# Performance work log

Measured on AMD Instinct MI355X. Metric: run time of the kernel, lower is better.

The kernel has to match this reference:

```python
import jax, jax.numpy as jnp
import numpy as np

B, N, Q, D, H = 8, 2048, 256, 1024, 16
HD = D // H


def setup_inputs() -> dict:
    key = jax.random.key(0)
    ks = jax.random.split(key, 6)
    scale = 1.0 / np.sqrt(D)
    return {
        "sources": jax.random.normal(ks[0], (B, N, D), dtype=jnp.float32),
        "queries": jax.random.normal(ks[1], (B, Q, D), dtype=jnp.float32),
        "w_in": jax.random.normal(ks[2], (3 * D, D), dtype=jnp.float32) * scale,
        "b_in": jax.random.normal(ks[3], (3 * D,), dtype=jnp.float32) * 0.02,
        "w_out": jax.random.normal(ks[4], (D, D), dtype=jnp.float32) * scale,
        "b_out": jax.random.normal(ks[5], (D,), dtype=jnp.float32) * 0.02,
    }


def reference(sources, queries, w_in, b_in, w_out, b_out):
    # torch nn.MultiheadAttention (batch_first, eval mode, no attn_mask),
    # applied per-sample with equal lengths == one batched cross-attention.
    w_q, w_k, w_v = jnp.split(w_in, 3, axis=0)   # each [D, D]
    b_q, b_k, b_v = jnp.split(b_in, 3, axis=0)
    q = queries @ w_q.T + b_q                    # [B, Q, D]
    k = sources @ w_k.T + b_k                    # [B, N, D]
    v = sources @ w_v.T + b_v                    # [B, N, D]
    q = q.reshape(B, Q, H, HD)
    k = k.reshape(B, N, H, HD)
    v = v.reshape(B, N, H, HD)
    scale = 1.0 / np.sqrt(HD).astype(np.float32)
    scores = jnp.einsum("bqhd,bkhd->bhqk", q, k) * scale  # [B, H, Q, N]
    attn = jax.nn.softmax(scores, axis=-1)
    out = jnp.einsum("bhqk,bkhd->bqhd", attn, v).reshape(B, Q, D)
    out = out @ w_out.T + b_out                  # out_proj
    return out + queries                         # residual (fix=False: no norm)
```

## Files before the change

### kernel.cpp

```cpp
#include <hip/hip_runtime.h>
#include <hip/hip_bf16.h>


typedef unsigned short u16;
typedef __attribute__((ext_vector_type(8))) short short8;
typedef __attribute__((ext_vector_type(4))) float floatx4;

static_assert(sizeof(short8) == 16, "short8 must be 16B");

__device__ __forceinline__ u16 f2bf(float f) {
  unsigned int x = __float_as_uint(f);
  x += 0x7fffu + ((x >> 16) & 1u);
  return (u16)(x >> 16);
}

__device__ __forceinline__ void gload16(const u16* g, u16* lds) {
  __builtin_amdgcn_global_load_lds(
      (const __attribute__((address_space(1))) unsigned int*)g,
      (__attribute__((address_space(3))) unsigned int*)lds, 16, 0, 0);
}

template <int N> __device__ __forceinline__ void vmwait() {
  if constexpr (N == 0)      asm volatile("s_waitcnt vmcnt(0)" ::: "memory");
  else if constexpr (N == 4) asm volatile("s_waitcnt vmcnt(4)" ::: "memory");
  else if constexpr (N == 6) asm volatile("s_waitcnt vmcnt(6)" ::: "memory");
  else if constexpr (N == 8) asm volatile("s_waitcnt vmcnt(8)" ::: "memory");
  else static_assert(N == 0, "unsupported vmcnt immediate");
}

__device__ __forceinline__ void lgkm0() {
  asm volatile("s_waitcnt lgkmcnt(0)" ::: "memory");
}

__device__ __forceinline__ void sfence() { __builtin_amdgcn_sched_barrier(0); }

__global__ __launch_bounds__(256) void f2bf_multi(
    const float* __restrict__ s, u16* __restrict__ so,
    const float* __restrict__ q, u16* __restrict__ qo,
    const float* __restrict__ wi, u16* __restrict__ wio,
    const float* __restrict__ wo, u16* __restrict__ woo) {
  int i = blockIdx.x * 256 + threadIdx.x;
  const float* in; u16* out; int idx;
  if (i < 4194304)      { in = s;  out = so;  idx = i; }
  else if (i < 4718592) { in = q;  out = qo;  idx = i - 4194304; }
  else if (i < 5505024) { in = wi; out = wio; idx = i - 4718592; }
  else if (i < 5767168) { in = wo; out = woo; idx = i - 5505024; }
  else return;
  float4 v = reinterpret_cast<const float4*>(in)[idx];
  ushort4 o;
  o.x = f2bf(v.x); o.y = f2bf(v.y); o.z = f2bf(v.z); o.w = f2bf(v.w);
  reinterpret_cast<ushort4*>(out)[idx] = o;
}

template <int MT, int NT>
__device__ __forceinline__ void gemm_core(
    const u16* __restrict__ A, int lda,
    const u16* __restrict__ Bm, int ldb, int K,
    u16* __restrict__ Alds, u16* __restrict__ Blds,
    floatx4 (&acc)[MT][NT]) {
  const int t = threadIdx.x;
  const int wave = t >> 6, lane = t & 63;
  const int rr = lane & 15, kq = lane >> 4;
  constexpr int AI = MT, BI = NT;
  constexpr int AELEMS = MT * 32 * 64;
  constexpr int BELEMS = NT * 32 * 64;

  const u16* ag[AI]; u16* al[AI];
#pragma unroll
  for (int i = 0; i < AI; ++i) {
    int s = i * 256 + t;
    int row = s >> 3, c16 = s & 7;
    ag[i] = A + (size_t)row * lda + ((c16 ^ (row & 7)) * 8);
    al[i] = Alds + (size_t)(i * 256 + wave * 64) * 8;
  }
  const u16* bg[BI]; u16* blp[BI];
#pragma unroll
  for (int i = 0; i < BI; ++i) {
    int s = i * 256 + t;
    int row = s >> 3, c16 = s & 7;
    bg[i] = Bm + (size_t)row * ldb + ((c16 ^ (row & 7)) * 8);
    blp[i] = Blds + (size_t)(i * 256 + wave * 64) * 8;
  }

  const int m0w = (wave & 1) * (MT * 16);
  const int n0w = (wave >> 1) * (NT * 16);
  int aoff[MT][2], boff[NT][2];
#pragma unroll
  for (int mi = 0; mi < MT; ++mi) {
    int row = m0w + mi * 16 + rr;
#pragma unroll
    for (int kk = 0; kk < 2; ++kk)
      aoff[mi][kk] = row * 64 + (((kk * 4 + kq) ^ (row & 7)) * 8);
  }
#pragma unroll
  for (int ni = 0; ni < NT; ++ni) {
    int row = n0w + ni * 16 + rr;
#pragma unroll
    for (int kk = 0; kk < 2; ++kk)
      boff[ni][kk] = row * 64 + (((kk * 4 + kq) ^ (row & 7)) * 8);
  }

  auto compute = [&](int bs) {
    const u16* Ab = Alds + bs * AELEMS;
    const u16* Bb = Blds + bs * BELEMS;
#pragma unroll
    for (int kk = 0; kk < 2; ++kk) {
      short8 af[MT], bfr[NT];
#pragma unroll
      for (int mi = 0; mi < MT; ++mi)
        af[mi] = *reinterpret_cast<const short8*>(Ab + aoff[mi][kk]);
#pragma unroll
      for (int ni = 0; ni < NT; ++ni)
        bfr[ni] = *reinterpret_cast<const short8*>(Bb + boff[ni][kk]);
      __builtin_amdgcn_s_setprio(1);
#pragma unroll
      for (int mi = 0; mi < MT; ++mi)
#pragma unroll
        for (int ni = 0; ni < NT; ++ni)
          acc[mi][ni] = __builtin_amdgcn_mfma_f32_16x16x32_bf16(af[mi], bfr[ni], acc[mi][ni], 0, 0, 0);
      __builtin_amdgcn_s_setprio(0);
    }
  };

  const int nt = K >> 6;

#pragma unroll
  for (int i = 0; i < AI; ++i) gload16(ag[i], al[i]);
#pragma unroll
  for (int i = 0; i < BI; ++i) gload16(bg[i], blp[i]);

  int cur = 0;
#pragma unroll 1
  for (int tt = 0; tt < nt - 1; ++tt) {
    const int nxt = cur ^ 1;
    const int koff = (tt + 1) * 64;
#pragma unroll
    for (int i = 0; i < AI; ++i) gload16(ag[i] + koff, al[i] + nxt * AELEMS);
#pragma unroll
    for (int i = 0; i < BI; ++i) gload16(bg[i] + koff, blp[i] + nxt * BELEMS);
    sfence();
    vmwait<AI + BI>();
    __builtin_amdgcn_s_barrier();
    sfence();
    compute(cur);
    sfence();
    __builtin_amdgcn_s_barrier();
    cur = nxt;
  }
  sfence();
  vmwait<0>();
  __builtin_amdgcn_s_barrier();
  sfence();
  compute(cur);
}


template <int LO>
__device__ __forceinline__ void read_a8(const u16* ab, int kcol0, int kcol1,
                                        short8 (&af)[8][2]) {
#pragma unroll
  for (int mi = 0; mi < 4; ++mi) {
    af[LO + mi][0] = *reinterpret_cast<const short8*>(ab + (LO + mi) * 1024 + kcol0);
    af[LO + mi][1] = *reinterpret_cast<const short8*>(ab + (LO + mi) * 1024 + kcol1);
  }
}

template <int LO>
__device__ __forceinline__ void read_b8(const u16* bb, int kcol0, int kcol1,
                                        short8 (&bf)[4][2]) {
#pragma unroll
  for (int ni = 0; ni < 2; ++ni) {
    bf[LO + ni][0] = *reinterpret_cast<const short8*>(bb + (LO + ni) * 1024 + kcol0);
    bf[LO + ni][1] = *reinterpret_cast<const short8*>(bb + (LO + ni) * 1024 + kcol1);
  }
}

template <int M0, int N0>
__device__ __forceinline__ void quad8(const short8 (&af)[8][2], const short8 (&bf)[4][2],
                                      floatx4 (&acc)[8][4]) {
  __builtin_amdgcn_s_setprio(1);
#pragma unroll
  for (int kk = 0; kk < 2; ++kk)
#pragma unroll
    for (int mi = 0; mi < 4; ++mi)
#pragma unroll
      for (int ni = 0; ni < 2; ++ni)
        acc[M0 + mi][N0 + ni] = __builtin_amdgcn_mfma_f32_16x16x32_bf16(
            af[M0 + mi][kk], bf[N0 + ni][kk], acc[M0 + mi][N0 + ni], 0, 0, 0);
  __builtin_amdgcn_s_setprio(0);
}

__global__ __launch_bounds__(512, 2) void gemm_proj_kv8(
    const u16* __restrict__ s_bf, const u16* __restrict__ wi_bf,
    const float* __restrict__ b_in,
    u16* __restrict__ kp, u16* __restrict__ vT) {
  __shared__ __attribute__((aligned(16))) u16 Alds[2 * 256 * 64];
  __shared__ __attribute__((aligned(16))) u16 Blds[2 * 256 * 64];

  int bid = blockIdx.y * 8 + blockIdx.x;
  int nb = (bid & 7) * 64 + (bid >> 3);
  const int by = nb >> 3, bx = nb & 7;
  const int mB = by * 256;
  const int nB = bx * 256;
  const u16* Ag = s_bf + (size_t)mB * 1024;
  const u16* Wg = wi_bf + (size_t)(1024 + nB) * 1024;
  const float* bias = b_in + 1024 + nB;

  const int t = threadIdx.x;
  const int w = t >> 6, lane = t & 63;
  const int rr = lane & 15, kq = lane >> 4;
  const int wr = w >> 2, wc = w & 3;

  const u16* ga[2][2]; const u16* gb[2][2];
#pragma unroll
  for (int h = 0; h < 2; ++h)
#pragma unroll
    for (int i = 0; i < 2; ++i) {
      int s = i * 512 + t;
      int row = h * 128 + (s >> 3), c16 = s & 7;
      ga[h][i] = Ag + (size_t)row * 1024 + ((c16 ^ (row & 7)) * 8);
      gb[h][i] = Wg + (size_t)row * 1024 + ((c16 ^ (row & 7)) * 8);
    }

#define STAGE_A8(j, h) { const int d_ = ((j) & 1) * 16384;                         \
    gload16(ga[h][0] + (size_t)(j) * 64, Alds + d_ + (h) * 8192 + w * 512);        \
    gload16(ga[h][1] + (size_t)(j) * 64, Alds + d_ + (h) * 8192 + 4096 + w * 512); }
#define STAGE_B8(j, h) { const int d_ = ((j) & 1) * 16384;                         \
    gload16(gb[h][0] + (size_t)(j) * 64, Blds + d_ + (h) * 8192 + w * 512);        \
    gload16(gb[h][1] + (size_t)(j) * 64, Blds + d_ + (h) * 8192 + 4096 + w * 512); }

  const int kcol0 = ((kq) ^ (rr & 7)) * 8;
  const int kcol1 = ((4 + kq) ^ (rr & 7)) * 8;
  const u16* abase = Alds + (wr * 128 + rr) * 64;
  const u16* bbase = Blds + (wc * 64 + rr) * 64;

  short8 af[8][2], bf[4][2];
  const floatx4 zz = {0.f, 0.f, 0.f, 0.f};
  floatx4 acc[8][4];
#pragma unroll
  for (int mi = 0; mi < 8; ++mi)
#pragma unroll
    for (int ni = 0; ni < 4; ++ni) acc[mi][ni] = zz;

  STAGE_A8(0, 0); STAGE_B8(0, 0); STAGE_A8(0, 1); STAGE_B8(0, 1);
  STAGE_A8(1, 0); STAGE_B8(1, 0);
  sfence();
  vmwait<4>();
  __builtin_amdgcn_s_barrier();
  sfence();

#pragma unroll 1
  for (int kt = 0; kt < 16; ++kt) {
    const int doff = (kt & 1) * 16384;
    const u16* ab = abase + doff;
    const u16* bb = bbase + doff;
    read_a8<0>(ab, kcol0, kcol1, af);
    read_b8<0>(bb, kcol0, kcol1, bf);
    if (kt + 1 < 16) STAGE_A8(kt + 1, 1);
    sfence();
    __builtin_amdgcn_s_barrier();
    lgkm0(); sfence();
    quad8<0, 0>(af, bf, acc);
    sfence();
    __builtin_amdgcn_s_barrier();
    sfence();
    read_a8<4>(ab, kcol0, kcol1, af);
    read_b8<2>(bb, kcol0, kcol1, bf);
    if (kt + 1 < 16) STAGE_B8(kt + 1, 1);
    sfence();
    __builtin_amdgcn_s_barrier();
    lgkm0(); sfence();
    quad8<0, 2>(af, bf, acc);
    sfence();
    __builtin_amdgcn_s_barrier();
    sfence();
    if (kt + 2 < 16) STAGE_A8(kt + 2, 0);
    sfence();
    __builtin_amdgcn_s_barrier();
    quad8<4, 0>(af, bf, acc);
    sfence();
    __builtin_amdgcn_s_barrier();
    sfence();
    if (kt + 2 < 16) { STAGE_B8(kt + 2, 0); sfence(); vmwait<4>(); }
    else             { sfence(); vmwait<0>(); }
    __builtin_amdgcn_s_barrier();
    quad8<4, 2>(af, bf, acc);
    sfence();
    __builtin_amdgcn_s_barrier();
    sfence();
  }
#undef STAGE_A8
#undef STAGE_B8

  const int r4 = kq * 4;
  const int m0w = wr * 128, n0w = wc * 64;
  if (nB < 1024) {
#pragma unroll
    for (int mi = 0; mi < 8; ++mi)
#pragma unroll
      for (int ni = 0; ni < 4; ++ni) {
        int nl = n0w + ni * 16 + rr;
        float bv = bias[nl];
#pragma unroll
        for (int r = 0; r < 4; ++r) {
          int m = mB + m0w + mi * 16 + r4 + r;
          kp[(size_t)m * 1024 + nB + nl] = f2bf(acc[mi][ni][r] + bv);
        }
      }
  } else {
#pragma unroll
    for (int mi = 0; mi < 8; ++mi)
#pragma unroll
      for (int ni = 0; ni < 4; ++ni) {
        int n2 = nB + n0w + ni * 16 + rr - 1024;
        int h = n2 >> 6, d = n2 & 63;
        float bv = bias[n0w + ni * 16 + rr];
        int m0 = mB + m0w + mi * 16 + r4;
        int b = m0 >> 11, j0 = m0 & 2047;
        ushort4 o;
        o.x = f2bf(acc[mi][ni][0] + bv);
        o.y = f2bf(acc[mi][ni][1] + bv);
        o.z = f2bf(acc[mi][ni][2] + bv);
        o.w = f2bf(acc[mi][ni][3] + bv);
        *reinterpret_cast<ushort4*>(
            vT + ((size_t)(b * 16 + h) * 64 + d) * 2048 + j0) = o;
      }
  }
}

__global__ __launch_bounds__(256, 2) void gemm_proj_q(
    const u16* __restrict__ qy_bf, const u16* __restrict__ wi_bf,
    const float* __restrict__ b_in, u16* __restrict__ qp) {
  __shared__ __attribute__((aligned(16))) u16 Alds[2 * 128 * 64];
  __shared__ __attribute__((aligned(16))) u16 Blds[2 * 128 * 64];
  const int mB = blockIdx.y * 128;
  const int nB = blockIdx.x * 128;
  const u16* A = qy_bf + (size_t)mB * 1024;
  const u16* W = wi_bf + (size_t)nB * 1024;
  const float* bias = b_in + nB;

  const floatx4 zz = {0.f, 0.f, 0.f, 0.f};
  floatx4 acc[4][4] = {{zz, zz, zz, zz}, {zz, zz, zz, zz}, {zz, zz, zz, zz}, {zz, zz, zz, zz}};
  gemm_core<4, 4>(A, 1024, W, 1024, 1024, Alds, Blds, acc);

  const int lane = threadIdx.x & 63, wave = threadIdx.x >> 6;
  const int rr = lane & 15, r4 = (lane >> 4) * 4;
  const int m0w = (wave & 1) * 64, n0w = (wave >> 1) * 64;
#pragma unroll
  for (int mi = 0; mi < 4; ++mi)
#pragma unroll
    for (int ni = 0; ni < 4; ++ni) {
      int nl = n0w + ni * 16 + rr;
      float bv = bias[nl];
#pragma unroll
      for (int r = 0; r < 4; ++r) {
        int m = mB + m0w + mi * 16 + r4 + r;
        qp[(size_t)m * 1024 + nB + nl] = f2bf((acc[mi][ni][r] + bv) * 0.125f);
      }
    }
}

__global__ __launch_bounds__(256, 2) void gemm_scores_exp(
    const u16* __restrict__ qp, const u16* __restrict__ kp,
    u16* __restrict__ sc, int b0) {
  __shared__ __attribute__((aligned(16))) u16 Alds[128 * 64];
  __shared__ __attribute__((aligned(16))) u16 Blds[128 * 64];
  const int bz = blockIdx.z, bl = bz >> 4, h = bz & 15;
  const int b = b0 + bl;
  const int mB = blockIdx.y * 128;
  const int nB = blockIdx.x * 128;
  const u16* A = qp + (size_t)b * 256 * 1024 + h * 64 + (size_t)mB * 1024;
  const u16* Bm = kp + (size_t)b * 2048 * 1024 + h * 64 + (size_t)nB * 1024;
  u16* C = sc + (size_t)bz * 256 * 2048;
  const floatx4 zz = {0.f, 0.f, 0.f, 0.f};
  floatx4 acc[4][4] = {{zz, zz, zz, zz}, {zz, zz, zz, zz}, {zz, zz, zz, zz}, {zz, zz, zz, zz}};
  gemm_core<4, 4>(A, 1024, Bm, 1024, 64, Alds, Blds, acc);

  const int lane = threadIdx.x & 63, wave = threadIdx.x >> 6;
  const int rr = lane & 15, r4 = (lane >> 4) * 4;
  const int m0w = (wave & 1) * 64, n0w = (wave >> 1) * 64;
#pragma unroll
  for (int mi = 0; mi < 4; ++mi)
#pragma unroll
    for (int ni = 0; ni < 4; ++ni) {
      int n = nB + n0w + ni * 16 + rr;
#pragma unroll
      for (int r = 0; r < 4; ++r) {
        int m = mB + m0w + mi * 16 + r4 + r;
        C[(size_t)m * 2048 + n] = f2bf(__expf(acc[mi][ni][r]));
      }
    }
}

__global__ __launch_bounds__(256, 2) void gemm_pv(
    const u16* __restrict__ sc, const u16* __restrict__ vT,
    u16* __restrict__ ao, int b0) {
  __shared__ __attribute__((aligned(16))) u16 Alds[2 * 64 * 64];
  __shared__ __attribute__((aligned(16))) u16 Blds[2 * 64 * 64];
  const int t = threadIdx.x;
  const int wave = t >> 6, lane = t & 63;
  const int rr = lane & 15, kq = lane >> 4;
  const int bz = blockIdx.z, bl = bz >> 4, h = bz & 15;
  const int b = b0 + bl;
  const int mB = blockIdx.y * 64;
  const u16* A = sc + (size_t)bz * 256 * 2048 + (size_t)mB * 2048;
  const u16* Bm = vT + (size_t)(b * 16 + h) * 64 * 2048;

  const u16* ag[2]; u16* al[2]; const u16* bg[2]; u16* blp[2];
#pragma unroll
  for (int i = 0; i < 2; ++i) {
    int s = i * 256 + t, row = s >> 3, c16 = s & 7;
    ag[i] = A + (size_t)row * 2048 + ((c16 ^ (row & 7)) * 8);
    al[i] = Alds + (size_t)(i * 256 + wave * 64) * 8;
    bg[i] = Bm + (size_t)row * 2048 + ((c16 ^ (row & 7)) * 8);
    blp[i] = Blds + (size_t)(i * 256 + wave * 64) * 8;
  }

  const int m0w = (wave & 1) * 32;
  const int n0w = (wave >> 1) * 32;
  int aoff[2][2], boff[2][2];
#pragma unroll
  for (int mi = 0; mi < 2; ++mi) {
    int row = m0w + mi * 16 + rr;
#pragma unroll
    for (int kk = 0; kk < 2; ++kk)
      aoff[mi][kk] = row * 64 + (((kk * 4 + kq) ^ (row & 7)) * 8);
  }
#pragma unroll
  for (int ni = 0; ni < 2; ++ni) {
    int row = n0w + ni * 16 + rr;
#pragma unroll
    for (int kk = 0; kk < 2; ++kk)
      boff[ni][kk] = row * 64 + (((kk * 4 + kq) ^ (row & 7)) * 8);
  }

  const short ov = (rr == 0) ? (short)0x3F80 : (short)0;
  const short8 ones = {ov, ov, ov, ov, ov, ov, ov, ov};

  const floatx4 zz = {0.f, 0.f, 0.f, 0.f};
  floatx4 acc[2][2] = {{zz, zz}, {zz, zz}};
  floatx4 acc_l[2] = {zz, zz};

  auto compute = [&](int bs) {
    const u16* Ab = Alds + bs * 4096;
    const u16* Bb = Blds + bs * 4096;
#pragma unroll
    for (int kk = 0; kk < 2; ++kk) {
      short8 af[2], bfr[2];
#pragma unroll
      for (int mi = 0; mi < 2; ++mi)
        af[mi] = *reinterpret_cast<const short8*>(Ab + aoff[mi][kk]);
#pragma unroll
      for (int ni = 0; ni < 2; ++ni)
        bfr[ni] = *reinterpret_cast<const short8*>(Bb + boff[ni][kk]);
      __builtin_amdgcn_s_setprio(1);
#pragma unroll
      for (int mi = 0; mi < 2; ++mi) {
#pragma unroll
        for (int ni = 0; ni < 2; ++ni)
          acc[mi][ni] = __builtin_amdgcn_mfma_f32_16x16x32_bf16(af[mi], bfr[ni], acc[mi][ni], 0, 0, 0);
        acc_l[mi] = __builtin_amdgcn_mfma_f32_16x16x32_bf16(af[mi], ones, acc_l[mi], 0, 0, 0);
      }
      __builtin_amdgcn_s_setprio(0);
    }
  };

#pragma unroll
  for (int i = 0; i < 2; ++i) gload16(ag[i], al[i]);
#pragma unroll
  for (int i = 0; i < 2; ++i) gload16(bg[i], blp[i]);

  int cur = 0;
#pragma unroll 1
  for (int tt = 0; tt < 31; ++tt) {
    const int nxt = cur ^ 1;
    const int koff = (tt + 1) * 64;
#pragma unroll
    for (int i = 0; i < 2; ++i) gload16(ag[i] + koff, al[i] + nxt * 4096);
#pragma unroll
    for (int i = 0; i < 2; ++i) gload16(bg[i] + koff, blp[i] + nxt * 4096);
    sfence();
    vmwait<4>();
    __builtin_amdgcn_s_barrier();
    sfence();
    compute(cur);
    sfence();
    __builtin_amdgcn_s_barrier();
    cur = nxt;
  }
  sfence();
  vmwait<0>();
  __builtin_amdgcn_s_barrier();
  sfence();
  compute(cur);

#pragma unroll
  for (int mi = 0; mi < 2; ++mi)
#pragma unroll
    for (int r = 0; r < 4; ++r) {
      float l = __shfl(acc_l[mi][r], lane & 48, 64);
      float inv = 1.0f / l;
      int m = mB + m0w + mi * 16 + kq * 4 + r;
#pragma unroll
      for (int ni = 0; ni < 2; ++ni) {
        int n = n0w + ni * 16 + rr;
        ao[(size_t)(b * 256 + m) * 1024 + h * 64 + n] = f2bf(acc[mi][ni][r] * inv);
      }
    }
}

__global__ __launch_bounds__(256, 2) void gemm_out(
    const u16* __restrict__ A, const u16* __restrict__ W,
    const float* __restrict__ bias, const float* __restrict__ resid,
    float* __restrict__ out) {
  __shared__ __attribute__((aligned(16))) u16 Alds[2 * 64 * 64];
  __shared__ __attribute__((aligned(16))) u16 Blds[2 * 128 * 64];
  const int mB = blockIdx.y * 64;
  const int nB = blockIdx.x * 128;
  const floatx4 zz = {0.f, 0.f, 0.f, 0.f};
  floatx4 acc[2][4] = {{zz, zz, zz, zz}, {zz, zz, zz, zz}};
  gemm_core<2, 4>(A + (size_t)mB * 1024, 1024, W + (size_t)nB * 1024, 1024, 1024,
                  Alds, Blds, acc);
  const int lane = threadIdx.x & 63, wave = threadIdx.x >> 6;
  const int rr = lane & 15, r4 = (lane >> 4) * 4;
  const int m0w = (wave & 1) * 32, n0w = (wave >> 1) * 64;
#pragma unroll
  for (int mi = 0; mi < 2; ++mi)
#pragma unroll
    for (int ni = 0; ni < 4; ++ni) {
      int n = nB + n0w + ni * 16 + rr;
      float bv = bias[n];
#pragma unroll
      for (int r = 0; r < 4; ++r) {
        int m = mB + m0w + mi * 16 + r4 + r;
        size_t idx = (size_t)m * 1024 + n;
        out[idx] = acc[mi][ni][r] + bv + resid[idx];
      }
    }
}

extern "C" void kernel_launch(void* const* d_in, const int* in_sizes, int n_in,
                              void* d_out, int out_size, void* d_ws, size_t ws_size,
                              hipStream_t stream) {
  const float* sources = (const float*)d_in[0];
  const float* queries = (const float*)d_in[1];
  const float* w_in    = (const float*)d_in[2];
  const float* b_in    = (const float*)d_in[3];
  const float* w_out   = (const float*)d_in[4];
  const float* b_out   = (const float*)d_in[5];
  float* out = (float*)d_out;

  char* ws = (char*)d_ws;
  size_t off = 0;
  auto alloc = [&](size_t elems) -> u16* {
    u16* p = (u16*)(ws + off);
    off += elems * sizeof(u16);
    off = (off + 255) & ~(size_t)255;
    return p;
  };
  u16* s_bf  = alloc((size_t)16777216);
  u16* qy_bf = alloc((size_t)2097152);
  u16* wi_bf = alloc((size_t)3145728);
  u16* wo_bf = alloc((size_t)1048576);
  u16* qp    = alloc((size_t)2097152);
  u16* kp    = alloc((size_t)16777216);
  u16* vT    = alloc((size_t)16777216);
  u16* ao    = alloc((size_t)2097152);
  const size_t sc_elems_per_b = (size_t)16 * 256 * 2048;
  size_t remain = ws_size > off ? ws_size - off : 0;
  int bchunk = (int)(remain / (sc_elems_per_b * sizeof(u16)));
  if (bchunk > 8) bchunk = 8;
  if (bchunk < 1) bchunk = 1;
  u16* sc = (u16*)(ws + off);

  f2bf_multi<<<dim3(22528), 256, 0, stream>>>(
      sources, s_bf, queries, qy_bf, w_in, wi_bf, w_out, wo_bf);

  gemm_proj_kv8<<<dim3(8, 64), 512, 0, stream>>>(s_bf, wi_bf, b_in, kp, vT);
  gemm_proj_q<<<dim3(8, 16), 256, 0, stream>>>(qy_bf, wi_bf, b_in, qp);

  for (int b0 = 0; b0 < 8; b0 += bchunk) {
    int nb = (8 - b0) < bchunk ? (8 - b0) : bchunk;
    gemm_scores_exp<<<dim3(16, 2, nb * 16), 256, 0, stream>>>(qp, kp, sc, b0);
    gemm_pv<<<dim3(1, 4, nb * 16), 256, 0, stream>>>(sc, vT, ao, b0);
  }

  gemm_out<<<dim3(8, 32), 256, 0, stream>>>(ao, wo_bf, b_out, queries, out);
}
```

Measured before the change: 314.6 us.

## Fuse scores-exp and PV GEMMs into one flash-style attention kernel

Replaces the separate score+exp kernel and the PV kernel, which went through a large bf16 score buffer in global memory, with a single fused kernel. Each block handles a (batch, head, 128-query) tile and streams K/V tiles through double-buffered LDS. Exponentiated scores are staged in LDS and consumed directly by the PV MFMAs, and row sums are reduced across waves at the end. This removes the global write and read of the score matrix and a kernel launch, but keeps the unnormalized exp without max subtraction and leaves only 256 blocks of 512 threads.

```diff
diff --git a/kernel.cpp b/kernel.cpp
--- a/kernel.cpp
+++ b/kernel.cpp
@@ -12,6 +12,10 @@
   unsigned int x = __float_as_uint(f);
   x += 0x7fffu + ((x >> 16) & 1u);
   return (u16)(x >> 16);
+}
+
+__device__ __forceinline__ float bf2f(u16 b) {
+  return __uint_as_float(((unsigned int)b) << 16);
 }
 
 __device__ __forceinline__ void gload16(const u16* g, u16* lds) {
@@ -154,7 +158,6 @@
   compute(cur);
 }
 
-
 template <int LO>
 __device__ __forceinline__ void read_a8(const u16* ab, int kcol0, int kcol1,
                                         short8 (&af)[8][2]) {
@@ -360,151 +363,201 @@
     }
 }
 
-__global__ __launch_bounds__(256, 2) void gemm_scores_exp(
+__global__ __launch_bounds__(512, 2) void attn_fused(
     const u16* __restrict__ qp, const u16* __restrict__ kp,
-    u16* __restrict__ sc, int b0) {
-  __shared__ __attribute__((aligned(16))) u16 Alds[128 * 64];
-  __shared__ __attribute__((aligned(16))) u16 Blds[128 * 64];
-  const int bz = blockIdx.z, bl = bz >> 4, h = bz & 15;
-  const int b = b0 + bl;
-  const int mB = blockIdx.y * 128;
-  const int nB = blockIdx.x * 128;
-  const u16* A = qp + (size_t)b * 256 * 1024 + h * 64 + (size_t)mB * 1024;
-  const u16* Bm = kp + (size_t)b * 2048 * 1024 + h * 64 + (size_t)nB * 1024;
-  u16* C = sc + (size_t)bz * 256 * 2048;
+    const u16* __restrict__ vT, u16* __restrict__ ao) {
+  __shared__ __attribute__((aligned(16))) u16 Qlds[8192];
+  __shared__ __attribute__((aligned(16))) u16 Klds[2][8192];
+  __shared__ __attribute__((aligned(16))) u16 Vlds[2][8192];
+  __shared__ __attribute__((aligned(16))) u16 Plds[16384];
+  __shared__ float l_part[4][128];
+
+  const int bid = blockIdx.x;
+  const int nb = (bid & 7) * 32 + (bid >> 3);
+  const int bh = nb >> 1, qh = nb & 1;
+  const int b = bh >> 4, h = bh & 15;
+
+  const int t = threadIdx.x;
+  const int w = t >> 6, lane = t & 63;
+  const int rr = lane & 15, kq = lane >> 4;
+  const int swz = rr & 7;
+  const int wrS = w >> 2, wcS = w & 3;
+  const int wrP = w >> 1, wcP = w & 1;
+
+  const u16* qg[2]; const u16* kg[2]; const u16* vg[2];
+  {
+    const u16* qbase = qp + ((size_t)(b * 256 + qh * 128)) * 1024 + h * 64;
+    const u16* kbase = kp + ((size_t)b * 2048) * 1024 + h * 64;
+    const u16* vbase = vT + ((size_t)bh * 64) * 2048;
+#pragma unroll
+    for (int i = 0; i < 2; ++i) {
+      int s = i * 512 + t;
+      int r8 = s >> 3, c8 = s & 7;
+      int r16 = s >> 4, c16 = s & 15;
+      qg[i] = qbase + (size_t)r8 * 1024 + ((c8 ^ (r8 & 7)) * 8);
+      kg[i] = kbase + (size_t)r8 * 1024 + ((c8 ^ (r8 & 7)) * 8);
+      vg[i] = vbase + (size_t)r16 * 2048 + ((c16 ^ (r16 & 7)) * 8);
+    }
+  }
+
+  float l_acc[4][4];
+#pragma unroll
+  for (int mi = 0; mi < 4; ++mi)
+#pragma unroll
+    for (int r = 0; r < 4; ++r) l_acc[mi][r] = 0.f;
   const floatx4 zz = {0.f, 0.f, 0.f, 0.f};
-  floatx4 acc[4][4] = {{zz, zz, zz, zz}, {zz, zz, zz, zz}, {zz, zz, zz, zz}, {zz, zz, zz, zz}};
-  gemm_core<4, 4>(A, 1024, Bm, 1024, 64, Alds, Blds, acc);
-
-  const int lane = threadIdx.x & 63, wave = threadIdx.x >> 6;
-  const int rr = lane & 15, r4 = (lane >> 4) * 4;
-  const int m0w = (wave & 1) * 64, n0w = (wave >> 1) * 64;
-#pragma unroll
-  for (int mi = 0; mi < 4; ++mi)
-#pragma unroll
-    for (int ni = 0; ni < 4; ++ni) {
-      int n = nB + n0w + ni * 16 + rr;
-#pragma unroll
-      for (int r = 0; r < 4; ++r) {
-        int m = mB + m0w + mi * 16 + r4 + r;
-        C[(size_t)m * 2048 + n] = f2bf(__expf(acc[mi][ni][r]));
-      }
-    }
-}
-
-__global__ __launch_bounds__(256, 2) void gemm_pv(
-    const u16* __restrict__ sc, const u16* __restrict__ vT,
-    u16* __restrict__ ao, int b0) {
-  __shared__ __attribute__((aligned(16))) u16 Alds[2 * 64 * 64];
-  __shared__ __attribute__((aligned(16))) u16 Blds[2 * 64 * 64];
-  const int t = threadIdx.x;
-  const int wave = t >> 6, lane = t & 63;
-  const int rr = lane & 15, kq = lane >> 4;
-  const int bz = blockIdx.z, bl = bz >> 4, h = bz & 15;
-  const int b = b0 + bl;
-  const int mB = blockIdx.y * 64;
-  const u16* A = sc + (size_t)bz * 256 * 2048 + (size_t)mB * 2048;
-  const u16* Bm = vT + (size_t)(b * 16 + h) * 64 * 2048;
-
-  const u16* ag[2]; u16* al[2]; const u16* bg[2]; u16* blp[2];
-#pragma unroll
-  for (int i = 0; i < 2; ++i) {
-    int s = i * 256 + t, row = s >> 3, c16 = s & 7;
-    ag[i] = A + (size_t)row * 2048 + ((c16 ^ (row & 7)) * 8);
-    al[i] = Alds + (size_t)(i * 256 + wave * 64) * 8;
-    bg[i] = Bm + (size_t)row * 2048 + ((c16 ^ (row & 7)) * 8);
-    blp[i] = Blds + (size_t)(i * 256 + wave * 64) * 8;
-  }
-
-  const int m0w = (wave & 1) * 32;
-  const int n0w = (wave >> 1) * 32;
-  int aoff[2][2], boff[2][2];
-#pragma unroll
-  for (int mi = 0; mi < 2; ++mi) {
-    int row = m0w + mi * 16 + rr;
-#pragma unroll
-    for (int kk = 0; kk < 2; ++kk)
-      aoff[mi][kk] = row * 64 + (((kk * 4 + kq) ^ (row & 7)) * 8);
-  }
-#pragma unroll
-  for (int ni = 0; ni < 2; ++ni) {
-    int row = n0w + ni * 16 + rr;
-#pragma unroll
-    for (int kk = 0; kk < 2; ++kk)
-      boff[ni][kk] = row * 64 + (((kk * 4 + kq) ^ (row & 7)) * 8);
-  }
-
-  const short ov = (rr == 0) ? (short)0x3F80 : (short)0;
-  const short8 ones = {ov, ov, ov, ov, ov, ov, ov, ov};
-
-  const floatx4 zz = {0.f, 0.f, 0.f, 0.f};
-  floatx4 acc[2][2] = {{zz, zz}, {zz, zz}};
-  floatx4 acc_l[2] = {zz, zz};
-
-  auto compute = [&](int bs) {
-    const u16* Ab = Alds + bs * 4096;
-    const u16* Bb = Blds + bs * 4096;
-#pragma unroll
-    for (int kk = 0; kk < 2; ++kk) {
-      short8 af[2], bfr[2];
-#pragma unroll
-      for (int mi = 0; mi < 2; ++mi)
-        af[mi] = *reinterpret_cast<const short8*>(Ab + aoff[mi][kk]);
-#pragma unroll
-      for (int ni = 0; ni < 2; ++ni)
-        bfr[ni] = *reinterpret_cast<const short8*>(Bb + boff[ni][kk]);
-      __builtin_amdgcn_s_setprio(1);
-#pragma unroll
-      for (int mi = 0; mi < 2; ++mi) {
-#pragma unroll
-        for (int ni = 0; ni < 2; ++ni)
-          acc[mi][ni] = __builtin_amdgcn_mfma_f32_16x16x32_bf16(af[mi], bfr[ni], acc[mi][ni], 0, 0, 0);
-        acc_l[mi] = __builtin_amdgcn_mfma_f32_16x16x32_bf16(af[mi], ones, acc_l[mi], 0, 0, 0);
-      }
-      __builtin_amdgcn_s_setprio(0);
-    }
-  };
-
-#pragma unroll
-  for (int i = 0; i < 2; ++i) gload16(ag[i], al[i]);
-#pragma unroll
-  for (int i = 0; i < 2; ++i) gload16(bg[i], blp[i]);
-
-  int cur = 0;
-#pragma unroll 1
-  for (int tt = 0; tt < 31; ++tt) {
-    const int nxt = cur ^ 1;
-    const int koff = (tt + 1) * 64;
-#pragma unroll
-    for (int i = 0; i < 2; ++i) gload16(ag[i] + koff, al[i] + nxt * 4096);
-#pragma unroll
-    for (int i = 0; i < 2; ++i) gload16(bg[i] + koff, blp[i] + nxt * 4096);
-    sfence();
-    vmwait<4>();
-    __builtin_amdgcn_s_barrier();
-    sfence();
-    compute(cur);
-    sfence();
-    __builtin_amdgcn_s_barrier();
-    cur = nxt;
-  }
+  floatx4 oacc[2][2] = {{zz, zz}, {zz, zz}};
+
+  ((float*)l_part)[t] = 0.f;
+#pragma unroll
+  for (int i = 0; i < 2; ++i) gload16(qg[i], Qlds + (i * 512 + w * 64) * 8);
+#pragma unroll
+  for (int i = 0; i < 2; ++i) gload16(kg[i], &Klds[0][(i * 512 + w * 64) * 8]);
+#pragma unroll
+  for (int i = 0; i < 2; ++i) gload16(vg[i], &Vlds[0][(i * 512 + w * 64) * 8]);
   sfence();
   vmwait<0>();
   __builtin_amdgcn_s_barrier();
   sfence();
-  compute(cur);
-
+
+  short8 qf[4][2];
+#pragma unroll
+  for (int mi = 0; mi < 4; ++mi) {
+    int qrow = wrS * 64 + mi * 16 + rr;
+#pragma unroll
+    for (int kc = 0; kc < 2; ++kc)
+      qf[mi][kc] = *reinterpret_cast<const short8*>(
+          Qlds + qrow * 64 + (((kc * 4 + kq) ^ swz) * 8));
+  }
+
+#pragma unroll 1
+  for (int kt = 0; kt < 16; ++kt) {
+    const int buf = kt & 1;
+    if (kt) { sfence(); __builtin_amdgcn_s_barrier(); sfence(); }
+    if (kt < 15) {
+      const int nxt = buf ^ 1;
+      const size_t ko = (size_t)(kt + 1) * 131072;
+      const size_t vo = (size_t)(kt + 1) * 128;
+#pragma unroll
+      for (int i = 0; i < 2; ++i) gload16(kg[i] + ko, &Klds[nxt][(i * 512 + w * 64) * 8]);
+#pragma unroll
+      for (int i = 0; i < 2; ++i) gload16(vg[i] + vo, &Vlds[nxt][(i * 512 + w * 64) * 8]);
+      sfence();
+      vmwait<4>();
+    } else {
+      sfence();
+      vmwait<0>();
+    }
+    short8 kf[2][2];
+#pragma unroll
+    for (int ni = 0; ni < 2; ++ni) {
+      int krow = wcS * 32 + ni * 16 + rr;
+#pragma unroll
+      for (int kc = 0; kc < 2; ++kc)
+        kf[ni][kc] = *reinterpret_cast<const short8*>(
+            &Klds[buf][krow * 64 + (((kc * 4 + kq) ^ swz) * 8)]);
+    }
+    lgkm0(); sfence();
+    floatx4 sacc[4][2];
+#pragma unroll
+    for (int mi = 0; mi < 4; ++mi)
+#pragma unroll
+      for (int ni = 0; ni < 2; ++ni) sacc[mi][ni] = zz;
+    __builtin_amdgcn_s_setprio(1);
+#pragma unroll
+    for (int kc = 0; kc < 2; ++kc)
+#pragma unroll
+      for (int mi = 0; mi < 4; ++mi)
+#pragma unroll
+        for (int ni = 0; ni < 2; ++ni)
+          sacc[mi][ni] = __builtin_amdgcn_mfma_f32_16x16x32_bf16(
+              qf[mi][kc], kf[ni][kc], sacc[mi][ni], 0, 0, 0);
+    __builtin_amdgcn_s_setprio(0);
+    sfence();
+#pragma unroll
+    for (int mi = 0; mi < 4; ++mi) {
+#pragma unroll
+      for (int r = 0; r < 4; ++r) {
+        int qr = wrS * 64 + mi * 16 + kq * 4 + r;
+        int rb = qr * 128;
+        int qsw = qr & 7;
+        float lsum = 0.f;
+#pragma unroll
+        for (int ni = 0; ni < 2; ++ni) {
+          int key = wcS * 32 + ni * 16 + rr;
+          u16 pb = f2bf(__expf(sacc[mi][ni][r]));
+          Plds[rb + ((((key >> 3) ^ qsw)) << 3) + (key & 7)] = pb;
+          lsum += bf2f(pb);
+        }
+        l_acc[mi][r] += lsum;
+      }
+    }
+    lgkm0();
+    sfence();
+    __builtin_amdgcn_s_barrier();
+    sfence();
+    short8 pa[2][4], vf[2][4];
+#pragma unroll
+    for (int mi = 0; mi < 2; ++mi) {
+      int qrow = wrP * 32 + mi * 16 + rr;
+#pragma unroll
+      for (int kc = 0; kc < 4; ++kc)
+        pa[mi][kc] = *reinterpret_cast<const short8*>(
+            Plds + qrow * 128 + ((((kc * 4 + kq) ^ swz)) << 3));
+    }
+#pragma unroll
+    for (int ni = 0; ni < 2; ++ni) {
+      int drow = wcP * 32 + ni * 16 + rr;
+#pragma unroll
+      for (int kc = 0; kc < 4; ++kc)
+        vf[ni][kc] = *reinterpret_cast<const short8*>(
+            &Vlds[buf][drow * 128 + ((((kc * 4 + kq) ^ swz)) << 3)]);
+    }
+    lgkm0(); sfence();
+    __builtin_amdgcn_s_setprio(1);
+#pragma unroll
+    for (int kc = 0; kc < 4; ++kc)
+#pragma unroll
+      for (int mi = 0; mi < 2; ++mi)
+#pragma unroll
+        for (int ni = 0; ni < 2; ++ni)
+          oacc[mi][ni] = __builtin_amdgcn_mfma_f32_16x16x32_bf16(
+              pa[mi][kc], vf[ni][kc], oacc[mi][ni], 0, 0, 0);
+    __builtin_amdgcn_s_setprio(0);
+    sfence();
+  }
+
+#pragma unroll
+  for (int mi = 0; mi < 4; ++mi)
+#pragma unroll
+    for (int r = 0; r < 4; ++r) {
+      float v = l_acc[mi][r];
+      v += __shfl_xor(v, 1, 64);
+      v += __shfl_xor(v, 2, 64);
+      v += __shfl_xor(v, 4, 64);
+      v += __shfl_xor(v, 8, 64);
+      l_acc[mi][r] = v;
+    }
+  if (rr == 0) {
+#pragma unroll
+    for (int mi = 0; mi < 4; ++mi)
+#pragma unroll
+      for (int r = 0; r < 4; ++r)
+        l_part[wcS][wrS * 64 + mi * 16 + kq * 4 + r] = l_acc[mi][r];
+  }
+  __syncthreads();
+
+  u16* aob = ao + ((size_t)(b * 256 + qh * 128)) * 1024 + h * 64;
 #pragma unroll
   for (int mi = 0; mi < 2; ++mi)
 #pragma unroll
     for (int r = 0; r < 4; ++r) {
-      float l = __shfl(acc_l[mi][r], lane & 48, 64);
-      float inv = 1.0f / l;
-      int m = mB + m0w + mi * 16 + kq * 4 + r;
+      int q = wrP * 32 + mi * 16 + kq * 4 + r;
+      float inv = 1.0f / (l_part[0][q] + l_part[1][q] + l_part[2][q] + l_part[3][q]);
 #pragma unroll
       for (int ni = 0; ni < 2; ++ni) {
-        int n = n0w + ni * 16 + rr;
-        ao[(size_t)(b * 256 + m) * 1024 + h * 64 + n] = f2bf(acc[mi][ni][r] * inv);
+        int d = wcP * 32 + ni * 16 + rr;
+        aob[(size_t)q * 1024 + d] = f2bf(oacc[mi][ni][r] * inv);
       }
     }
 }
@@ -566,12 +619,6 @@
   u16* kp    = alloc((size_t)16777216);
   u16* vT    = alloc((size_t)16777216);
   u16* ao    = alloc((size_t)2097152);
-  const size_t sc_elems_per_b = (size_t)16 * 256 * 2048;
-  size_t remain = ws_size > off ? ws_size - off : 0;
-  int bchunk = (int)(remain / (sc_elems_per_b * sizeof(u16)));
-  if (bchunk > 8) bchunk = 8;
-  if (bchunk < 1) bchunk = 1;
-  u16* sc = (u16*)(ws + off);
 
   f2bf_multi<<<dim3(22528), 256, 0, stream>>>(
       sources, s_bf, queries, qy_bf, w_in, wi_bf, w_out, wo_bf);
@@ -579,11 +626,7 @@
   gemm_proj_kv8<<<dim3(8, 64), 512, 0, stream>>>(s_bf, wi_bf, b_in, kp, vT);
   gemm_proj_q<<<dim3(8, 16), 256, 0, stream>>>(qy_bf, wi_bf, b_in, qp);
 
-  for (int b0 = 0; b0 < 8; b0 += bchunk) {
-    int nb = (8 - b0) < bchunk ? (8 - b0) : bchunk;
-    gemm_scores_exp<<<dim3(16, 2, nb * 16), 256, 0, stream>>>(qp, kp, sc, b0);
-    gemm_pv<<<dim3(1, 4, nb * 16), 256, 0, stream>>>(sc, vT, ao, b0);
-  }
+  attn_fused<<<dim3(256), 512, 0, stream>>>(qp, kp, vT, ao);
 
   gemm_out<<<dim3(8, 32), 256, 0, stream>>>(ao, wo_bf, b_out, queries, out);
 }
```

Result: faster. 275.8 us (-12.3%).
